# Kernel optimization log

Measured on AMD Instinct MI355X. Metric: run time of the kernel, lower is better.

## Reference

```python
import jax, jax.numpy as jnp
import numpy as np


def setup_inputs() -> dict:
    key = jax.random.key(0)
    k1, k2 = jax.random.split(key)
    B, L, D = 16, 512, 256
    text_features = jax.random.normal(k1, (B, L, D), dtype=jnp.float32)
    durations = jax.random.randint(k2, (B, L), 0, 32, dtype=jnp.int64)
    return {"text_features": text_features, "durations": durations, "target_length": 8192}


def reference(text_features, durations, target_length):
    """Length-regulator: expand [B,L,d] phoneme features to [B,T,d] frames.

    Frame t of batch b copies phoneme p where cumsum(dur)[b,p-1] <= t < cumsum(dur)[b,p];
    frames past the total duration are zero (matches torch zeros-init + trim/pad to
    target_length, since padding with the last frame only occurs when the buffer was
    already target_length long in the original code path with target_length set).
    """
    B, L, D = text_features.shape
    T = target_length  # static python int -> jit-friendly fixed output length
    cum = jnp.cumsum(durations, axis=1)                      # [B, L]
    t = jnp.arange(T, dtype=cum.dtype)                       # [T]
    # first phoneme index p with cum[b,p] > t  (side='right')
    idx = jax.vmap(lambda c: jnp.searchsorted(c, t, side='right'))(cum)  # [B, T]
    idx = jnp.minimum(idx, L - 1)
    valid = t[None, :] < cum[:, -1:]                         # [B, T] frames within total dur
    gathered = jnp.take_along_axis(text_features, idx[:, :, None], axis=1)  # [B, T, D]
    return jnp.where(valid[:, :, None], gathered, jnp.zeros((), dtype=text_features.dtype))
```

## Files before the change

### kernel.cpp

```cpp
#include <hip/hip_runtime.h>

#define MAX_L 2048
#define FRAMES_PER_BLOCK 64

__global__ void lr_cumsum_kernel(const int* __restrict__ dur,
                                 int* __restrict__ cum,
                                 const int* __restrict__ tlen,
                                 int BL, int BT) {
    const int T = *tlen;
    const int B = BT / T;
    const int L = BL / B;
    __shared__ int s[MAX_L];
    for (int b = blockIdx.x; b < B; b += gridDim.x) {
        for (int i = threadIdx.x; i < L; i += blockDim.x)
            s[i] = dur[b * L + i];
        __syncthreads();
        for (int off = 1; off < L; off <<= 1) {
            int tmp[MAX_L / 256];
            int c = 0;
            for (int i = threadIdx.x; i < L; i += blockDim.x)
                tmp[c++] = (i >= off) ? (s[i] + s[i - off]) : s[i];
            __syncthreads();
            c = 0;
            for (int i = threadIdx.x; i < L; i += blockDim.x)
                s[i] = tmp[c++];
            __syncthreads();
        }
        for (int i = threadIdx.x; i < L; i += blockDim.x)
            cum[b * L + i] = s[i];
        __syncthreads();
    }
}

__global__ __launch_bounds__(256) void lr_expand_kernel(
        const float* __restrict__ feat,
        const int* __restrict__ cum,
        const int* __restrict__ tlen,
        float* __restrict__ out,
        int BL, int BT, int D) {
    const int T = *tlen;
    const int B = BT / T;
    const int L = BL / B;
    const int vecs = D >> 2;

    __shared__ int sc[MAX_L];
    __shared__ int sidx[FRAMES_PER_BLOCK];

    const int frame_base = blockIdx.x * FRAMES_PER_BLOCK;
    if (frame_base >= BT) return;
    const int b = frame_base / T;
    const int t0 = frame_base - b * T;

    const int* __restrict__ crow = cum + (size_t)b * L;
    for (int i = threadIdx.x; i < L; i += blockDim.x)
        sc[i] = crow[i];
    __syncthreads();

    const int total = sc[L - 1];

    if (threadIdx.x < FRAMES_PER_BLOCK) {
        const int t = t0 + threadIdx.x;
        int p = -1;
        if (t < total && frame_base + threadIdx.x < BT) {
            int lo = 0, hi = L - 1;
            while (lo < hi) {
                const int mid = (lo + hi) >> 1;
                if (sc[mid] > t) hi = mid;
                else             lo = mid + 1;
            }
            p = lo;
        }
        sidx[threadIdx.x] = p;
    }
    __syncthreads();

    const int wv   = threadIdx.x >> 6;
    const int lane = threadIdx.x & 63;
    const int fpw  = FRAMES_PER_BLOCK / 4;

    const float4* __restrict__ fbase = (const float4*)(feat + (size_t)b * L * D);
    float4* __restrict__ obase = (float4*)(out + (size_t)frame_base * D);
    const float4 z = make_float4(0.f, 0.f, 0.f, 0.f);

#pragma unroll 4
    for (int j = 0; j < fpw; ++j) {
        const int f = wv * fpw + j;
        if (frame_base + f >= BT) continue;
        const int p = sidx[f];
        float4* __restrict__ orow = obase + (size_t)f * vecs;
        if (p >= 0) {
            const float4* __restrict__ irow = fbase + (size_t)p * vecs;
            for (int i = lane; i < vecs; i += 64)
                orow[i] = irow[i];
        } else {
            for (int i = lane; i < vecs; i += 64)
                orow[i] = z;
        }
    }
}

extern "C" void kernel_launch(void* const* d_in, const int* in_sizes, int n_in,
                              void* d_out, int out_size, void* d_ws, size_t ws_size,
                              hipStream_t stream) {
    const float* feat = (const float*)d_in[0];
    const int*   dur  = (const int*)d_in[1];
    const int*   tlen = (const int*)d_in[2];

    const int BL = in_sizes[1];
    const int D  = in_sizes[0] / in_sizes[1];
    const int BT = out_size / D;

    int* cum = (int*)d_ws;

    lr_cumsum_kernel<<<64, 256, 0, stream>>>(dur, cum, tlen, BL, BT);

    const int grid = (BT + FRAMES_PER_BLOCK - 1) / FRAMES_PER_BLOCK;
    lr_expand_kernel<<<grid, 256, 0, stream>>>(feat, cum, tlen, (float*)d_out,
                                               BL, BT, D);
}
```

Baseline: 155.0 us.

## Fuse cumsum into expand kernel with per-block shuffle-based prefix scan

Removes the separate cumsum kernel and its launch. Each expand block now computes the prefix sum of its batch row itself, using per-thread serial sums, a wave shuffle scan and a cross-wave combine, instead of reading a precomputed cum array from workspace. The copy loop gets a specialized path for D=256 that fully unrolls 16 frames per wave, and launch bounds now request 3 blocks per CU. The trade-off is redundant scan work in every block (128 blocks per batch row) and extra duration reads, in exchange for one fewer launch and no dependency on the slow Hillis-Steele kernel.

```diff
diff --git a/kernel.cpp b/kernel.cpp
--- a/kernel.cpp
+++ b/kernel.cpp
@@ -1,40 +1,12 @@
 #include <hip/hip_runtime.h>
 
 #define MAX_L 2048
+#define MAX_EPC 8
 #define FRAMES_PER_BLOCK 64
 
-__global__ void lr_cumsum_kernel(const int* __restrict__ dur,
-                                 int* __restrict__ cum,
-                                 const int* __restrict__ tlen,
-                                 int BL, int BT) {
-    const int T = *tlen;
-    const int B = BT / T;
-    const int L = BL / B;
-    __shared__ int s[MAX_L];
-    for (int b = blockIdx.x; b < B; b += gridDim.x) {
-        for (int i = threadIdx.x; i < L; i += blockDim.x)
-            s[i] = dur[b * L + i];
-        __syncthreads();
-        for (int off = 1; off < L; off <<= 1) {
-            int tmp[MAX_L / 256];
-            int c = 0;
-            for (int i = threadIdx.x; i < L; i += blockDim.x)
-                tmp[c++] = (i >= off) ? (s[i] + s[i - off]) : s[i];
-            __syncthreads();
-            c = 0;
-            for (int i = threadIdx.x; i < L; i += blockDim.x)
-                s[i] = tmp[c++];
-            __syncthreads();
-        }
-        for (int i = threadIdx.x; i < L; i += blockDim.x)
-            cum[b * L + i] = s[i];
-        __syncthreads();
-    }
-}
-
-__global__ __launch_bounds__(256) void lr_expand_kernel(
+__global__ __launch_bounds__(256, 3) void lr_fused_kernel(
         const float* __restrict__ feat,
-        const int* __restrict__ cum,
+        const int* __restrict__ dur,
         const int* __restrict__ tlen,
         float* __restrict__ out,
         int BL, int BT, int D) {
@@ -44,24 +16,54 @@
     const int vecs = D >> 2;
 
     __shared__ int sc[MAX_L];
+    __shared__ int swsum[4];
     __shared__ int sidx[FRAMES_PER_BLOCK];
 
     const int frame_base = blockIdx.x * FRAMES_PER_BLOCK;
     if (frame_base >= BT) return;
-    const int b = frame_base / T;
+    const int b  = frame_base / T;
     const int t0 = frame_base - b * T;
 
-    const int* __restrict__ crow = cum + (size_t)b * L;
-    for (int i = threadIdx.x; i < L; i += blockDim.x)
-        sc[i] = crow[i];
+    const int tid  = threadIdx.x;
+    const int lane = tid & 63;
+    const int wv   = tid >> 6;
+
+    const int epc  = (L + blockDim.x - 1) / blockDim.x;
+    const int base = tid * epc;
+    const int* __restrict__ drow = dur + (size_t)b * L;
+
+    int local[MAX_EPC];
+    int run = 0;
+#pragma unroll
+    for (int e = 0; e < MAX_EPC; ++e) {
+        int v = 0;
+        if (e < epc && base + e < L) v = drow[base + e];
+        run += v;
+        local[e] = run;
+    }
+    int ws = run;
+#pragma unroll
+    for (int off = 1; off < 64; off <<= 1) {
+        int up = __shfl_up(ws, off, 64);
+        if (lane >= off) ws += up;
+    }
+    if (lane == 63) swsum[wv] = ws;
+    __syncthreads();
+    int wprefix = 0;
+    for (int w = 0; w < wv; ++w) wprefix += swsum[w];
+    const int chunk_prefix = wprefix + ws - run;
+#pragma unroll
+    for (int e = 0; e < MAX_EPC; ++e) {
+        if (e < epc && base + e < L) sc[base + e] = chunk_prefix + local[e];
+    }
     __syncthreads();
 
     const int total = sc[L - 1];
 
-    if (threadIdx.x < FRAMES_PER_BLOCK) {
-        const int t = t0 + threadIdx.x;
+    if (tid < FRAMES_PER_BLOCK) {
+        const int t = t0 + tid;
         int p = -1;
-        if (t < total && frame_base + threadIdx.x < BT) {
+        if (t < total && frame_base + tid < BT) {
             int lo = 0, hi = L - 1;
             while (lo < hi) {
                 const int mid = (lo + hi) >> 1;
@@ -70,31 +72,37 @@
             }
             p = lo;
         }
-        sidx[threadIdx.x] = p;
+        sidx[tid] = p;
     }
     __syncthreads();
 
-    const int wv   = threadIdx.x >> 6;
-    const int lane = threadIdx.x & 63;
-    const int fpw  = FRAMES_PER_BLOCK / 4;
-
-    const float4* __restrict__ fbase = (const float4*)(feat + (size_t)b * L * D);
-    float4* __restrict__ obase = (float4*)(out + (size_t)frame_base * D);
     const float4 z = make_float4(0.f, 0.f, 0.f, 0.f);
 
-#pragma unroll 4
-    for (int j = 0; j < fpw; ++j) {
-        const int f = wv * fpw + j;
-        if (frame_base + f >= BT) continue;
-        const int p = sidx[f];
-        float4* __restrict__ orow = obase + (size_t)f * vecs;
-        if (p >= 0) {
-            const float4* __restrict__ irow = fbase + (size_t)p * vecs;
-            for (int i = lane; i < vecs; i += 64)
-                orow[i] = irow[i];
-        } else {
-            for (int i = lane; i < vecs; i += 64)
-                orow[i] = z;
+    if (vecs == 64) {
+        const float4* __restrict__ fb = (const float4*)(feat + (size_t)b * L * D);
+        float4* __restrict__ ob = (float4*)(out + (size_t)frame_base * D);
+#pragma unroll
+        for (int j = 0; j < 16; ++j) {
+            const int f  = wv * 16 + j;
+            const int pj = sidx[f];
+            float4 v = z;
+            if (pj >= 0) v = fb[(size_t)pj * 64 + lane];
+            ob[(size_t)f * 64 + lane] = v;
+        }
+    } else {
+        const float4* __restrict__ fb = (const float4*)(feat + (size_t)b * L * D);
+        float4* __restrict__ ob = (float4*)(out + (size_t)frame_base * D);
+        for (int j = 0; j < 16; ++j) {
+            const int f = wv * 16 + j;
+            if (frame_base + f >= BT) continue;
+            const int pj = sidx[f];
+            float4* __restrict__ orow = ob + (size_t)f * vecs;
+            if (pj >= 0) {
+                const float4* __restrict__ irow = fb + (size_t)pj * vecs;
+                for (int i = lane; i < vecs; i += 64) orow[i] = irow[i];
+            } else {
+                for (int i = lane; i < vecs; i += 64) orow[i] = z;
+            }
         }
     }
 }
@@ -110,11 +118,7 @@
     const int D  = in_sizes[0] / in_sizes[1];
     const int BT = out_size / D;
 
-    int* cum = (int*)d_ws;
-
-    lr_cumsum_kernel<<<64, 256, 0, stream>>>(dur, cum, tlen, BL, BT);
-
     const int grid = (BT + FRAMES_PER_BLOCK - 1) / FRAMES_PER_BLOCK;
-    lr_expand_kernel<<<grid, 256, 0, stream>>>(feat, cum, tlen, (float*)d_out,
-                                               BL, BT, D);
+    lr_fused_kernel<<<grid, 256, 0, stream>>>(feat, dur, tlen, (float*)d_out,
+                                              BL, BT, D);
 }
```

Result: faster. 147.8 us (-4.6%).
